# Kernel optimization log

Measured on AMD Instinct MI355X. Metric: run time of the kernel, lower is better.

The kernel has to match this reference:

```python
import jax, jax.numpy as jnp
import numpy as np

DIM = 128
SUPPORT = 1
NL, NM, NG = 5, 20, 100
EPS_BN = 1e-5
EPS_NORM = 1e-12


def knn_idx(vertices, k):
    # vertices: (b, v, 3) -> (b, v, k) indices of k nearest (excluding self)
    sq = jnp.sum(vertices * vertices, axis=-1)  # (b, v)
    dist = -2.0 * jnp.einsum('bic,bjc->bij', vertices, vertices) + sq[:, :, None] + sq[:, None, :]
    _, idx = jax.lax.top_k(-dist, k + 1)  # smallest distances
    return idx[:, :, 1:]


def gather_nbr(t, idx):
    # t: (b, v, c), idx: (b, v, n) -> (b, v, n, c)
    b = t.shape[0]
    return t[jnp.arange(b)[:, None, None], idx]


def conv_layer(idx, vertices, fmap, W, bias, dirs):
    # idx: (b,v,n); fmap: (b,v,DIM); W: (DIM,(S+1)*DIM); bias: ((S+1)*DIM,); dirs: (3,S*DIM)
    nbrs = gather_nbr(vertices, idx)                      # (b,v,n,3)
    d = nbrs - vertices[:, :, None, :]
    d = d / jnp.maximum(jnp.linalg.norm(d, axis=-1, keepdims=True), EPS_NORM)
    sd = dirs / jnp.maximum(jnp.linalg.norm(dirs, axis=0, keepdims=True), EPS_NORM)
    theta = jax.nn.relu(jnp.einsum('bvnc,ck->bvnk', d, sd))  # (b,v,n,S*DIM)
    fo = fmap @ W + bias                                   # (b,v,(S+1)*DIM)
    center = fo[..., :DIM]
    supp = gather_nbr(fo[..., DIM:], idx)                  # (b,v,n,S*DIM)
    b_, v_, n_ = idx.shape
    act = (theta * supp).reshape(b_, v_, n_, SUPPORT, DIM)
    act = jnp.max(act, axis=2).sum(axis=2)                 # max over neighbors, sum over supports
    return center + act                                    # (b,v,DIM)


def bn_relu(x, gamma, beta):
    # training-mode BatchNorm1d over (batch, points) per channel, then ReLU
    mu = jnp.mean(x, axis=(0, 1))
    var = jnp.var(x, axis=(0, 1))
    return jax.nn.relu((x - mu) * jax.lax.rsqrt(var + EPS_BN) * gamma + beta)


def setup_inputs() -> dict:
    key = jax.random.key(0)
    ks = jax.random.split(key, 8)
    B, V = 2, 1024
    return {
        'vertices': jax.random.normal(ks[0], (B, V, 3), jnp.float32),
        'x': jax.random.normal(ks[1], (B, V, DIM), jnp.float32),
        'conv_W': jax.random.normal(ks[2], (6, DIM, (SUPPORT + 1) * DIM), jnp.float32) * 0.05,
        'conv_b': jax.random.normal(ks[3], (6, (SUPPORT + 1) * DIM), jnp.float32) * 0.05,
        'conv_dirs': jax.random.normal(ks[4], (6, 3, SUPPORT * DIM), jnp.float32),
        'bn_gamma': jnp.ones((6, DIM), jnp.float32),
        'bn_beta': jnp.zeros((6, DIM), jnp.float32),
        'down_W': jax.random.normal(ks[5], (3 * DIM, 2 * DIM), jnp.float32) * 0.05,
        'down_b': jax.random.normal(ks[6], (2 * DIM,), jnp.float32) * 0.05,
    }


def reference(vertices, x, conv_W, conv_b, conv_dirs, bn_gamma, bn_beta, down_W, down_b):
    il = knn_idx(vertices, NL)
    im = knn_idx(vertices, NM)
    ig = knn_idx(vertices, NG)
    # param index order: 0=l, 1=m0, 2=m1, 3=g0, 4=g1, 5=g2 (g2 unused, per source bug)
    fl = bn_relu(conv_layer(il, vertices, x, conv_W[0], conv_b[0], conv_dirs[0]), bn_gamma[0], bn_beta[0])
    fm = bn_relu(conv_layer(im, vertices, x, conv_W[1], conv_b[1], conv_dirs[1]), bn_gamma[1], bn_beta[1])
    fm = bn_relu(conv_layer(im, vertices, fm, conv_W[2], conv_b[2], conv_dirs[2]), bn_gamma[2], bn_beta[2])
    fg = bn_relu(conv_layer(ig, vertices, x, conv_W[3], conv_b[3], conv_dirs[3]), bn_gamma[3], bn_beta[3])
    fg = bn_relu(conv_layer(ig, vertices, fg, conv_W[4], conv_b[4], conv_dirs[4]), bn_gamma[4], bn_beta[4])
    # source reuses conv_g0 / bn_g0 for the third global layer
    fg = bn_relu(conv_layer(ig, vertices, fg, conv_W[3], conv_b[3], conv_dirs[3]), bn_gamma[3], bn_beta[3])
    out = jnp.concatenate([fl, fm, fg], axis=2)            # (b, v, 3*DIM)
    return jax.nn.relu(out @ down_W + down_b)              # (b, v, 2*DIM)
```

## Files before the change

### kernel.cpp

```cpp
#include <hip/hip_runtime.h>


__device__ __forceinline__ void do_gemm(
    const float* __restrict__ in, const float* __restrict__ stp,
    const float* __restrict__ gm, const float* __restrict__ bt,
    const float* __restrict__ W, const float* __restrict__ bi,
    float* __restrict__ out, int rb, char* smemc)
{
    float* rows  = (float*)smemc;
    float* wch   = rows + 1024;
    float* scale = wch + 4096;
    float* shift = scale + 128;
    int t = threadIdx.x;
    if (t < 128) {
        float sc = 1.0f, sf = 0.0f;
        if (stp) {
            float sm = 0.0f, sq = 0.0f;
            #pragma unroll 8
            for (int bk = 0; bk < 32; ++bk) {
                sm += stp[bk*256 + t];
                sq += stp[bk*256 + 128 + t];
            }
            float mu  = sm * (1.0f/2048.0f);
            float var = sq * (1.0f/2048.0f) - mu*mu;
            sc = rsqrtf(var + 1e-5f) * gm[t];
            sf = bt[t] - mu*sc;
        }
        scale[t] = sc; shift[t] = sf;
    }
    __syncthreads();
    int r0 = rb * 8;
    {
        float4 v = ((const float4*)(in + r0*128))[t];
        if (stp) {
            int c4 = (t & 31) << 2;
            v.x = fmaxf(v.x*scale[c4  ] + shift[c4  ], 0.0f);
            v.y = fmaxf(v.y*scale[c4+1] + shift[c4+1], 0.0f);
            v.z = fmaxf(v.z*scale[c4+2] + shift[c4+2], 0.0f);
            v.w = fmaxf(v.w*scale[c4+3] + shift[c4+3], 0.0f);
        }
        ((float4*)rows)[t] = v;
    }
    int cb = t & 63, rp = (t >> 6) << 1;
    const float* a0r = rows + rp*128;
    const float* a1r = a0r + 128;
    const float4* W4 = (const float4*)W;
    float4* wch4 = (float4*)wch;
    float4 acc0 = make_float4(0.f,0.f,0.f,0.f);
    float4 acc1 = make_float4(0.f,0.f,0.f,0.f);
    for (int c = 0; c < 8; ++c) {
        __syncthreads();
        #pragma unroll
        for (int i = 0; i < 4; ++i)
            wch4[t + 256*i] = W4[c*1024 + t + 256*i];
        __syncthreads();
        int kb = c*16;
        #pragma unroll
        for (int k = 0; k < 16; k += 4) {
            float4 a0 = *(const float4*)(a0r + kb + k);
            float4 a1 = *(const float4*)(a1r + kb + k);
            float4 w;
            w = wch4[(k+0)*64+cb];
            acc0.x += a0.x*w.x; acc0.y += a0.x*w.y; acc0.z += a0.x*w.z; acc0.w += a0.x*w.w;
            acc1.x += a1.x*w.x; acc1.y += a1.x*w.y; acc1.z += a1.x*w.z; acc1.w += a1.x*w.w;
            w = wch4[(k+1)*64+cb];
            acc0.x += a0.y*w.x; acc0.y += a0.y*w.y; acc0.z += a0.y*w.z; acc0.w += a0.y*w.w;
            acc1.x += a1.y*w.x; acc1.y += a1.y*w.y; acc1.z += a1.y*w.z; acc1.w += a1.y*w.w;
            w = wch4[(k+2)*64+cb];
            acc0.x += a0.z*w.x; acc0.y += a0.z*w.y; acc0.z += a0.z*w.z; acc0.w += a0.z*w.w;
            acc1.x += a1.z*w.x; acc1.y += a1.z*w.y; acc1.z += a1.z*w.z; acc1.w += a1.z*w.w;
            w = wch4[(k+3)*64+cb];
            acc0.x += a0.w*w.x; acc0.y += a0.w*w.y; acc0.z += a0.w*w.z; acc0.w += a0.w*w.w;
            acc1.x += a1.w*w.x; acc1.y += a1.w*w.y; acc1.z += a1.w*w.z; acc1.w += a1.w*w.w;
        }
    }
    float4 b4 = ((const float4*)bi)[cb];
    acc0.x += b4.x; acc0.y += b4.y; acc0.z += b4.z; acc0.w += b4.w;
    acc1.x += b4.x; acc1.y += b4.y; acc1.z += b4.z; acc1.w += b4.w;
    ((float4*)out)[(r0+rp  )*64 + cb] = acc0;
    ((float4*)out)[(r0+rp+1)*64 + cb] = acc1;
}

__device__ __forceinline__ void do_gemm_big(
    const float* __restrict__ in, const float* __restrict__ stp,
    const float* __restrict__ gm, const float* __restrict__ bt,
    const float* __restrict__ W, const float* __restrict__ bi,
    float* __restrict__ out, int rb, char* smemc)
{
    float* rows  = (float*)smemc;
    float* wch   = rows + 1024;
    float* scale = wch + 16384;
    float* shift = scale + 128;
    int t = threadIdx.x;
    if (t < 128) {
        float sc = 1.0f, sf = 0.0f;
        if (stp) {
            float sm = 0.0f, sq = 0.0f;
            #pragma unroll 8
            for (int bk = 0; bk < 32; ++bk) {
                sm += stp[bk*256 + t];
                sq += stp[bk*256 + 128 + t];
            }
            float mu  = sm * (1.0f/2048.0f);
            float var = sq * (1.0f/2048.0f) - mu*mu;
            sc = rsqrtf(var + 1e-5f) * gm[t];
            sf = bt[t] - mu*sc;
        }
        scale[t] = sc; shift[t] = sf;
    }
    __syncthreads();
    int r0 = rb * 8;
    {
        float4 v = ((const float4*)(in + r0*128))[t];
        if (stp) {
            int c4 = (t & 31) << 2;
            v.x = fmaxf(v.x*scale[c4  ] + shift[c4  ], 0.0f);
            v.y = fmaxf(v.y*scale[c4+1] + shift[c4+1], 0.0f);
            v.z = fmaxf(v.z*scale[c4+2] + shift[c4+2], 0.0f);
            v.w = fmaxf(v.w*scale[c4+3] + shift[c4+3], 0.0f);
        }
        ((float4*)rows)[t] = v;
    }
    int cb = t & 63, rp = (t >> 6) << 1;
    const float* a0r = rows + rp*128;
    const float* a1r = a0r + 128;
    const float4* W4 = (const float4*)W;
    float4* wch4 = (float4*)wch;
    float4 acc0 = make_float4(0.f,0.f,0.f,0.f);
    float4 acc1 = make_float4(0.f,0.f,0.f,0.f);
    for (int c = 0; c < 2; ++c) {
        __syncthreads();
        #pragma unroll
        for (int i = 0; i < 16; ++i)
            wch4[t + 256*i] = W4[c*4096 + t + 256*i];
        __syncthreads();
        int kb = c*64;
        #pragma unroll 4
        for (int k = 0; k < 64; k += 4) {
            float4 a0 = *(const float4*)(a0r + kb + k);
            float4 a1 = *(const float4*)(a1r + kb + k);
            float4 w;
            w = wch4[(k+0)*64+cb];
            acc0.x += a0.x*w.x; acc0.y += a0.x*w.y; acc0.z += a0.x*w.z; acc0.w += a0.x*w.w;
            acc1.x += a1.x*w.x; acc1.y += a1.x*w.y; acc1.z += a1.x*w.z; acc1.w += a1.x*w.w;
            w = wch4[(k+1)*64+cb];
            acc0.x += a0.y*w.x; acc0.y += a0.y*w.y; acc0.z += a0.y*w.z; acc0.w += a0.y*w.w;
            acc1.x += a1.y*w.x; acc1.y += a1.y*w.y; acc1.z += a1.y*w.z; acc1.w += a1.y*w.w;
            w = wch4[(k+2)*64+cb];
            acc0.x += a0.z*w.x; acc0.y += a0.z*w.y; acc0.z += a0.z*w.z; acc0.w += a0.z*w.w;
            acc1.x += a1.z*w.x; acc1.y += a1.z*w.y; acc1.z += a1.z*w.z; acc1.w += a1.z*w.w;
            w = wch4[(k+3)*64+cb];
            acc0.x += a0.w*w.x; acc0.y += a0.w*w.y; acc0.z += a0.w*w.z; acc0.w += a0.w*w.w;
            acc1.x += a1.w*w.x; acc1.y += a1.w*w.y; acc1.z += a1.w*w.z; acc1.w += a1.w*w.w;
        }
    }
    float4 b4 = ((const float4*)bi)[cb];
    acc0.x += b4.x; acc0.y += b4.y; acc0.z += b4.z; acc0.w += b4.w;
    acc1.x += b4.x; acc1.y += b4.y; acc1.z += b4.z; acc1.w += b4.w;
    ((float4*)out)[(r0+rp  )*64 + cb] = acc0;
    ((float4*)out)[(r0+rp+1)*64 + cb] = acc1;
}

__global__ void k1_kernel(const float* __restrict__ verts, const float* __restrict__ dirs,
                          const float* __restrict__ x,
                          const float* __restrict__ convW, const float* __restrict__ convB,
                          int* __restrict__ idxout, float* __restrict__ sdn,
                          float* __restrict__ stp, float* __restrict__ fo)
{
    __shared__ __align__(16) char smem[21504];
    int t = threadIdx.x;
    int blk = blockIdx.x;

    if (blk >= 1280) {
        if (blk == 1472) {
            for (int i = t; i < 768; i += 256) {
                int l = i >> 7, k = i & 127;
                float a = dirs[l*384 + k];
                float b = dirs[l*384 + 128 + k];
                float c = dirs[l*384 + 256 + k];
                float nrm = sqrtf(a*a + b*b + c*c);
                float inv = 1.0f / fmaxf(nrm, 1e-12f);
                sdn[l*384 + k]       = a*inv;
                sdn[l*384 + 128 + k] = b*inv;
                sdn[l*384 + 256 + k] = c*inv;
            }
        } else {
            stp[(blk - 1280)*256 + t] = 0.0f;
        }
        return;
    }
    if (blk >= 512) {
        int g = blk - 512;
        int s = g >> 8, rb = g & 255;
        int wi = (s==0) ? 0 : (s==1) ? 1 : 3;
        do_gemm(x, (const float*)0, (const float*)0, (const float*)0,
                convW + wi*32768, convB + wi*256, fo + s*524288, rb, smem);
        return;
    }

    float* xs  = (float*)smem;
    float* ys  = xs + 1024;
    float* zs  = ys + 1024;
    float* sqs = zs + 1024;
    unsigned int* histBase = (unsigned int*)(smem + 16384);
    unsigned int* selBase  = (unsigned int*)(smem + 20480);

    int w = t >> 6, l = t & 63;
    int vglob = blk*4 + w;
    int b = vglob >> 10;
    int v = vglob & 1023;
    unsigned long long* keys = (unsigned long long*)smem + w*256;
    unsigned int* hist = histBase + w*256;
    unsigned int* sel  = selBase + w*4;

    const float* vb = verts + b * 3072;
    for (int i = t; i < 1024; i += 256) {
        float xx = vb[i*3+0], yy = vb[i*3+1], zz = vb[i*3+2];
        xs[i] = xx; ys[i] = yy; zs[i] = zz;
        sqs[i] = xx*xx + yy*yy + zz*zz;
    }
    __syncthreads();

    float cx = xs[v], cy = ys[v], cz = zs[v], csq = sqs[v];
    unsigned long long K16[16];
    #pragma unroll
    for (int q = 0; q < 16; ++q) {
        int j = q*64 + l;
        float dot = cx*xs[j] + cy*ys[j] + cz*zs[j];
        float d = -2.0f*dot + csq + sqs[j];
        unsigned int u = __float_as_uint(d);
        u = (u & 0x80000000u) ? ~u : (u | 0x80000000u);
        K16[q] = (((unsigned long long)u) << 32) | (unsigned long long)j;
    }
    #pragma unroll
    for (int i = 0; i < 4; ++i) hist[l*4 + i] = 0u;
    __syncthreads();

    #pragma unroll
    for (int q = 0; q < 16; ++q)
        atomicAdd(&hist[(unsigned int)(K16[q] >> 56)], 1u);
    __syncthreads();

    {
        unsigned int h0 = hist[l*4], h1 = hist[l*4+1], h2 = hist[l*4+2], h3 = hist[l*4+3];
        unsigned int c1 = h0, c2 = h0+h1, c3 = h0+h1+h2, T = c3+h3;
        unsigned int xacc = T;
        #pragma unroll
        for (int off = 1; off < 64; off <<= 1) {
            unsigned int y = __shfl_up(xacc, off, 64);
            if (l >= off) xacc += y;
        }
        unsigned int P = xacc - T;
        unsigned int ex[4] = {P, P+c1, P+c2, P+c3};
        unsigned int hh[4] = {h0, h1, h2, h3};
        #pragma unroll
        for (int i = 0; i < 4; ++i) {
            if (ex[i] < 101u && ex[i] + hh[i] >= 101u) {
                sel[0] = (unsigned int)(l*4 + i);
                sel[1] = 101u - ex[i];
            }
        }
    }
    __syncthreads();
    unsigned int P8 = sel[0], rank2 = sel[1];
    #pragma unroll
    for (int i = 0; i < 4; ++i) hist[l*4 + i] = 0u;
    __syncthreads();

    #pragma unroll
    for (int q = 0; q < 16; ++q)
        if ((unsigned int)(K16[q] >> 56) == P8)
            atomicAdd(&hist[(unsigned int)(K16[q] >> 48) & 0xFFu], 1u);
    __syncthreads();

    {
        unsigned int h0 = hist[l*4], h1 = hist[l*4+1], h2 = hist[l*4+2], h3 = hist[l*4+3];
        unsigned int c1 = h0, c2 = h0+h1, c3 = h0+h1+h2, T = c3+h3;
        unsigned int xacc = T;
        #pragma unroll
        for (int off = 1; off < 64; off <<= 1) {
            unsigned int y = __shfl_up(xacc, off, 64);
            if (l >= off) xacc += y;
        }
        unsigned int P = xacc - T;
        unsigned int ex[4] = {P, P+c1, P+c2, P+c3};
        unsigned int hh[4] = {h0, h1, h2, h3};
        #pragma unroll
        for (int i = 0; i < 4; ++i) {
            if (ex[i] < rank2 && ex[i] + hh[i] >= rank2) {
                sel[2] = (P8 << 8) | (unsigned int)(l*4 + i);
                sel[3] = 0u;
            }
        }
    }
    __syncthreads();
    unsigned int P16 = sel[2];

    #pragma unroll
    for (int q = 0; q < 16; ++q) {
        if ((unsigned int)(K16[q] >> 48) <= P16) {
            unsigned int pos = atomicAdd(&sel[3], 1u);
            if (pos < 256u) keys[pos] = K16[q];
        }
    }
    __syncthreads();
    unsigned int cnt = sel[3];

    unsigned long long K[4];
    #pragma unroll
    for (int q = 0; q < 4; ++q) {
        unsigned int e = (unsigned int)(l*4 + q);
        K[q] = (e < cnt) ? keys[e] : 0xFFFFFFFFFFFFFFFFULL;
    }

    auto cswap = [&](int qa, int qb, int k) {
        int e = (l << 2) + qa;
        bool up = ((e & k) == 0);
        unsigned long long a = K[qa], bb2 = K[qb];
        unsigned long long mn = a < bb2 ? a : bb2;
        unsigned long long mx = a < bb2 ? bb2 : a;
        K[qa] = up ? mn : mx;
        K[qb] = up ? mx : mn;
    };
    #pragma unroll
    for (int k = 2; k <= 256; k <<= 1) {
        for (int j = k >> 1; j >= 4; j >>= 1) {
            int lj = j >> 2;
            #pragma unroll
            for (int q = 0; q < 4; ++q) {
                unsigned long long other = __shfl_xor(K[q], lj, 64);
                int e = (l << 2) + q;
                bool up = ((e & k) == 0);
                bool lower = ((l & lj) == 0);
                bool takeMin = (lower == up);
                unsigned long long mn = K[q] < other ? K[q] : other;
                unsigned long long mx = K[q] < other ? other : K[q];
                K[q] = takeMin ? mn : mx;
            }
        }
        if (k >= 4) { cswap(0, 2, k); cswap(1, 3, k); }
        cswap(0, 1, k); cswap(2, 3, k);
    }

    #pragma unroll
    for (int q = 0; q < 4; ++q) {
        int e = l*4 + q;
        if (e >= 1 && e <= 100)
            idxout[vglob*100 + (e-1)] = (int)(K[q] & 0xFFFFFFFFu);
    }
}

__global__ void agg_kernel(const int* __restrict__ idx, const float* __restrict__ verts,
                           const float* __restrict__ sdn, const float* __restrict__ fo,
                           int n0, int n1, int n2, int d0, int d1, int d2,
                           float* o0, float* o1, float* o2,
                           float* s0p, float* s1p, float* s2p)
{
    __shared__ float4 ds4s[200];
    __shared__ int jss[200];
    int slot = blockIdx.y;
    int n  = slot==0 ? n0 : slot==1 ? n1 : n2;
    int dI = slot==0 ? d0 : slot==1 ? d1 : d2;
    float* outp = slot==0 ? o0 : slot==1 ? o1 : o2;
    float* stp  = slot==0 ? s0p : slot==1 ? s1p : s2p;
    const float* fos = fo + slot * 524288;
    const float* sd = sdn + dI * 384;

    int t = threadIdx.x;
    int h = t >> 7, tt = t & 127;
    float4* ds4 = ds4s + h*100;
    int* js = jss + h*100;
    int r = blockIdx.x*2 + h;
    int b = r >> 10;

    if (tt < n) {
        int j = idx[r*100 + tt];
        js[tt] = j;
        const float* pj = verts + (b*1024 + j)*3;
        const float* pv = verts + r*3;
        float dx = pj[0]-pv[0], dy = pj[1]-pv[1], dz = pj[2]-pv[2];
        float nm = sqrtf(dx*dx + dy*dy + dz*dz);
        float inv = 1.0f / fmaxf(nm, 1e-12f);
        ds4[tt] = make_float4(dx*inv, dy*inv, dz*inv, 0.0f);
    }
    __syncthreads();
    float s0 = sd[tt], s1 = sd[128+tt], s2 = sd[256+tt];
    int bb = b * 1024;
    float m = -3.0e38f;
    for (int q = 0; q < n; q += 5) {
        float th[5];
        const float* p[5];
        #pragma unroll
        for (int u = 0; u < 5; ++u) {
            float4 dq = ds4[q+u];
            th[u] = fmaxf(dq.x*s0 + dq.y*s1 + dq.z*s2, 0.0f);
            p[u] = fos + (size_t)(bb + js[q+u])*256 + 128 + tt;
        }
        float vv[5];
        #pragma unroll
        for (int u = 0; u < 5; ++u) vv[u] = *p[u];
        #pragma unroll
        for (int u = 0; u < 5; ++u) m = fmaxf(m, th[u]*vv[u]);
    }
    float val = fos[r*256 + tt] + m;
    outp[r*128 + tt] = val;
    float* bank = stp + (r & 31)*256;
    atomicAdd(&bank[tt], val);
    atomicAdd(&bank[128+tt], val*val);
}

__global__ void gemm2_kernel(
    const float* inA, const float* stA, const float* gA, const float* beA,
    const float* WA, const float* biA, float* foA,
    const float* inB, const float* stB, const float* gB, const float* beB,
    const float* WB, const float* biB, float* foB)
{
    __shared__ __align__(16) char smem[70656];
    if (blockIdx.y == 0)
        do_gemm_big(inA, stA, gA, beA, WA, biA, foA, blockIdx.x, smem);
    else
        do_gemm_big(inB, stB, gB, beB, WB, biB, foB, blockIdx.x, smem);
}

__global__ void down_kernel(
    const float* __restrict__ p0, const float* __restrict__ s0p,
    const float* __restrict__ g0, const float* __restrict__ be0,
    const float* __restrict__ p1, const float* __restrict__ s1p,
    const float* __restrict__ g1, const float* __restrict__ be1,
    const float* __restrict__ p2, const float* __restrict__ s2p,
    const float* __restrict__ g2, const float* __restrict__ be2,
    const float* __restrict__ dW, const float* __restrict__ db,
    float* __restrict__ out)
{
    __shared__ __align__(16) float rows[16*384];
    __shared__ __align__(16) float4 wch4[4096];
    __shared__ float scale[384], shift[384];
    int t = threadIdx.x;
    int r0 = blockIdx.x * 16;
    int colblk = blockIdx.y;

    for (int c = t; c < 384; c += 256) {
        int seg = c >> 7, cc = c & 127;
        const float* stp = seg==0 ? s0p : seg==1 ? s1p : s2p;
        const float* g   = seg==0 ? g0  : seg==1 ? g1  : g2;
        const float* be  = seg==0 ? be0 : seg==1 ? be1 : be2;
        float sm = 0.0f, sq = 0.0f;
        #pragma unroll 8
        for (int bk = 0; bk < 32; ++bk) {
            sm += stp[bk*256 + cc];
            sq += stp[bk*256 + 128 + cc];
        }
        float mu  = sm * (1.0f/2048.0f);
        float var = sq * (1.0f/2048.0f) - mu*mu;
        float s = rsqrtf(var + 1e-5f) * g[cc];
        scale[c] = s;
        shift[c] = be[cc] - mu*s;
    }
    __syncthreads();
    for (int q = t; q < 1536; q += 256) {
        int row = q / 96, rem = q - row*96;
        int c4 = rem << 2;
        int seg = c4 >> 7, cc = c4 & 127;
        const float* ps = seg==0 ? p0 : seg==1 ? p1 : p2;
        float4 v = *(const float4*)(ps + (r0+row)*128 + cc);
        v.x = fmaxf(v.x*scale[c4  ] + shift[c4  ], 0.0f);
        v.y = fmaxf(v.y*scale[c4+1] + shift[c4+1], 0.0f);
        v.z = fmaxf(v.z*scale[c4+2] + shift[c4+2], 0.0f);
        v.w = fmaxf(v.w*scale[c4+3] + shift[c4+3], 0.0f);
        *(float4*)&rows[row*384 + c4] = v;
    }

    int cb = t & 31;
    int rg = t >> 5;
    const float* a0r = rows + (rg*2)*384;
    const float* a1r = a0r + 384;
    const float4* W4 = (const float4*)dW;
    float4 acc0 = make_float4(0.f,0.f,0.f,0.f);
    float4 acc1 = make_float4(0.f,0.f,0.f,0.f);
    for (int c = 0; c < 3; ++c) {
        __syncthreads();
        #pragma unroll
        for (int i = 0; i < 16; ++i) {
            int e = t + 256*i;
            wch4[e] = W4[c*8192 + colblk*32 + (e >> 5)*64 + (e & 31)];
        }
        __syncthreads();
        int kb = c*128;
        #pragma unroll 8
        for (int k = 0; k < 128; k += 4) {
            float4 a0 = *(const float4*)(a0r + kb + k);
            float4 a1 = *(const float4*)(a1r + kb + k);
            float4 w;
            w = wch4[(k+0)*32+cb];
            acc0.x += a0.x*w.x; acc0.y += a0.x*w.y; acc0.z += a0.x*w.z; acc0.w += a0.x*w.w;
            acc1.x += a1.x*w.x; acc1.y += a1.x*w.y; acc1.z += a1.x*w.z; acc1.w += a1.x*w.w;
            w = wch4[(k+1)*32+cb];
            acc0.x += a0.y*w.x; acc0.y += a0.y*w.y; acc0.z += a0.y*w.z; acc0.w += a0.y*w.w;
            acc1.x += a1.y*w.x; acc1.y += a1.y*w.y; acc1.z += a1.y*w.z; acc1.w += a1.y*w.w;
            w = wch4[(k+2)*32+cb];
            acc0.x += a0.z*w.x; acc0.y += a0.z*w.y; acc0.z += a0.z*w.z; acc0.w += a0.z*w.w;
            acc1.x += a1.z*w.x; acc1.y += a1.z*w.y; acc1.z += a1.z*w.z; acc1.w += a1.z*w.w;
            w = wch4[(k+3)*32+cb];
            acc0.x += a0.w*w.x; acc0.y += a0.w*w.y; acc0.z += a0.w*w.z; acc0.w += a0.w*w.w;
            acc1.x += a1.w*w.x; acc1.y += a1.w*w.y; acc1.z += a1.w*w.z; acc1.w += a1.w*w.w;
        }
    }
    float4 b4 = ((const float4*)db)[colblk*32 + cb];
    float4 o0, o1;
    o0.x = fmaxf(acc0.x + b4.x, 0.0f); o0.y = fmaxf(acc0.y + b4.y, 0.0f);
    o0.z = fmaxf(acc0.z + b4.z, 0.0f); o0.w = fmaxf(acc0.w + b4.w, 0.0f);
    o1.x = fmaxf(acc1.x + b4.x, 0.0f); o1.y = fmaxf(acc1.y + b4.y, 0.0f);
    o1.z = fmaxf(acc1.z + b4.z, 0.0f); o1.w = fmaxf(acc1.w + b4.w, 0.0f);
    ((float4*)out)[(r0 + rg*2    )*64 + colblk*32 + cb] = o0;
    ((float4*)out)[(r0 + rg*2 + 1)*64 + colblk*32 + cb] = o1;
}

extern "C" void kernel_launch(void* const* d_in, const int* in_sizes, int n_in,
                              void* d_out, int out_size, void* d_ws, size_t ws_size,
                              hipStream_t stream)
{
    (void)in_sizes; (void)n_in; (void)out_size; (void)ws_size;
    const float* verts = (const float*)d_in[0];
    const float* x     = (const float*)d_in[1];
    const float* convW = (const float*)d_in[2];
    const float* convB = (const float*)d_in[3];
    const float* dirs  = (const float*)d_in[4];
    const float* gam   = (const float*)d_in[5];
    const float* bet   = (const float*)d_in[6];
    const float* dW    = (const float*)d_in[7];
    const float* db    = (const float*)d_in[8];
    float* out = (float*)d_out;

    char* ws = (char*)d_ws;
    int*   idxb = (int*)(ws);
    float* sdn  = (float*)(ws + 819200);
    float* stp  = (float*)(ws + 828416);
    float* fo   = (float*)(ws + 1025024);
    float* p0   = (float*)(ws + 7316480);
    float* p1   = (float*)(ws + 8365056);
    float* p2   = (float*)(ws + 9413632);
    float* p3   = (float*)(ws + 10462208);
    float* p4   = (float*)(ws + 11510784);
    float* p5   = (float*)(ws + 12559360);

    const float* nf = (const float*)0;
    float* nw = (float*)0;
    float* stL0 = stp,         *stL1 = stp + 8192, *stL2 = stp + 16384;
    float* stL3 = stp + 24576, *stL4 = stp + 32768, *stL5 = stp + 40960;

    k1_kernel<<<1473, 256, 0, stream>>>(verts, dirs, x, convW, convB,
                                        idxb, sdn, stp, fo);
    agg_kernel<<<dim3(1024,3), 256, 0, stream>>>(
        idxb, verts, sdn, fo, 5, 20, 100, 0, 1, 3,
        p0, p1, p3, stL0, stL1, stL3);
    gemm2_kernel<<<dim3(256,2), 256, 0, stream>>>(
        p1, stL1, gam + 128, bet + 128, convW + 65536,  convB + 512,  fo,
        p3, stL3, gam + 384, bet + 384, convW + 131072, convB + 1024, fo + 524288);
    agg_kernel<<<dim3(1024,2), 256, 0, stream>>>(
        idxb, verts, sdn, fo, 20, 100, 0, 2, 4, 0,
        p2, p4, nw, stL2, stL4, nw);
    gemm2_kernel<<<dim3(256,1), 256, 0, stream>>>(
        p4, stL4, gam + 512, bet + 512, convW + 98304, convB + 768, fo,
        nf, nf, nf, nf, nf, nf, nw);
    agg_kernel<<<dim3(1024,1), 256, 0, stream>>>(
        idxb, verts, sdn, fo, 100, 0, 0, 3, 0, 0,
        p5, nw, nw, stL5, nw, nw);
    down_kernel<<<dim3(128,2), 256, 0, stream>>>(
        p0, stL0, gam, bet,
        p2, stL2, gam + 256, bet + 256,
        p5, stL5, gam + 384, bet + 384,
        dW, db, out);
}
```

Measured before the change: 178.1 us.

## Vectorize neighbor gather with float4 and split neighbors across thread groups

The aggregation kernel now has each thread handle four channels through float4 loads and split the neighbor list across four groups of 32 threads. Partial maxima are combined through a shared-memory reduction. Neighbor offsets are precomputed as row*256 in shared memory. The aim is fewer, wider gather loads and more memory-level parallelism per thread, at the cost of an extra barrier, a shared reduction, and masked tail iterations when n is not a multiple of 20.

New measurement: 201.3 us. 13.1% more time.

```diff
diff --git a/kernel.cpp b/kernel.cpp
--- a/kernel.cpp
+++ b/kernel.cpp
@@ -358,6 +358,7 @@
 {
     __shared__ float4 ds4s[200];
     __shared__ int jss[200];
+    __shared__ float4 redm[2][4][32];
     int slot = blockIdx.y;
     int n  = slot==0 ? n0 : slot==1 ? n1 : n2;
     int dI = slot==0 ? d0 : slot==1 ? d1 : d2;
@@ -372,41 +373,83 @@
     int* js = jss + h*100;
     int r = blockIdx.x*2 + h;
     int b = r >> 10;
+    int bb = b * 1024;
 
     if (tt < n) {
         int j = idx[r*100 + tt];
-        js[tt] = j;
-        const float* pj = verts + (b*1024 + j)*3;
+        const float* pj = verts + (bb + j)*3;
         const float* pv = verts + r*3;
         float dx = pj[0]-pv[0], dy = pj[1]-pv[1], dz = pj[2]-pv[2];
         float nm = sqrtf(dx*dx + dy*dy + dz*dz);
         float inv = 1.0f / fmaxf(nm, 1e-12f);
         ds4[tt] = make_float4(dx*inv, dy*inv, dz*inv, 0.0f);
-    }
-    __syncthreads();
-    float s0 = sd[tt], s1 = sd[128+tt], s2 = sd[256+tt];
-    int bb = b * 1024;
-    float m = -3.0e38f;
-    for (int q = 0; q < n; q += 5) {
-        float th[5];
-        const float* p[5];
+        js[tt] = (bb + j) << 8;
+    }
+    __syncthreads();
+
+    int c = tt & 31, g = tt >> 5;
+    int c4 = c << 2;
+    float4 S0 = *(const float4*)(sd + c4);
+    float4 S1 = *(const float4*)(sd + 128 + c4);
+    float4 S2 = *(const float4*)(sd + 256 + c4);
+
+    float4 m4 = make_float4(-3.0e38f, -3.0e38f, -3.0e38f, -3.0e38f);
+    for (int q = g; q < n; q += 20) {
+        float4 th[5]; int off[5]; bool ok[5];
         #pragma unroll
         for (int u = 0; u < 5; ++u) {
-            float4 dq = ds4[q+u];
-            th[u] = fmaxf(dq.x*s0 + dq.y*s1 + dq.z*s2, 0.0f);
-            p[u] = fos + (size_t)(bb + js[q+u])*256 + 128 + tt;
-        }
-        float vv[5];
-        #pragma unroll
-        for (int u = 0; u < 5; ++u) vv[u] = *p[u];
-        #pragma unroll
-        for (int u = 0; u < 5; ++u) m = fmaxf(m, th[u]*vv[u]);
-    }
-    float val = fos[r*256 + tt] + m;
-    outp[r*128 + tt] = val;
-    float* bank = stp + (r & 31)*256;
-    atomicAdd(&bank[tt], val);
-    atomicAdd(&bank[128+tt], val*val);
+            int qq = q + u*4;
+            ok[u] = (qq < n);
+            int qs = ok[u] ? qq : g;
+            float4 dq = ds4[qs];
+            th[u].x = fmaxf(dq.x*S0.x + dq.y*S1.x + dq.z*S2.x, 0.0f);
+            th[u].y = fmaxf(dq.x*S0.y + dq.y*S1.y + dq.z*S2.y, 0.0f);
+            th[u].z = fmaxf(dq.x*S0.z + dq.y*S1.z + dq.z*S2.z, 0.0f);
+            th[u].w = fmaxf(dq.x*S0.w + dq.y*S1.w + dq.z*S2.w, 0.0f);
+            off[u] = js[qs];
+        }
+        float4 vv[5];
+        #pragma unroll
+        for (int u = 0; u < 5; ++u)
+            vv[u] = *(const float4*)(fos + off[u] + 128 + c4);
+        #pragma unroll
+        for (int u = 0; u < 5; ++u) {
+            if (ok[u]) {
+                m4.x = fmaxf(m4.x, th[u].x*vv[u].x);
+                m4.y = fmaxf(m4.y, th[u].y*vv[u].y);
+                m4.z = fmaxf(m4.z, th[u].z*vv[u].z);
+                m4.w = fmaxf(m4.w, th[u].w*vv[u].w);
+            }
+        }
+    }
+    redm[h][g][c] = m4;
+    __syncthreads();
+    if (g < 2) {
+        float4 aa = redm[h][0][c], bq = redm[h][1][c];
+        float4 cq = redm[h][2][c], dq2 = redm[h][3][c];
+        float4 mm;
+        mm.x = fmaxf(fmaxf(aa.x,bq.x), fmaxf(cq.x,dq2.x));
+        mm.y = fmaxf(fmaxf(aa.y,bq.y), fmaxf(cq.y,dq2.y));
+        mm.z = fmaxf(fmaxf(aa.z,bq.z), fmaxf(cq.z,dq2.z));
+        mm.w = fmaxf(fmaxf(aa.w,bq.w), fmaxf(cq.w,dq2.w));
+        float4 ctr = *(const float4*)(fos + r*256 + c4);
+        float4 val;
+        val.x = ctr.x + mm.x; val.y = ctr.y + mm.y;
+        val.z = ctr.z + mm.z; val.w = ctr.w + mm.w;
+        if (g == 0) {
+            *(float4*)(outp + r*128 + c4) = val;
+        } else {
+            float* bank = stp + (r & 31)*256;
+            atomicAdd(&bank[c4+0], val.x);
+            atomicAdd(&bank[c4+1], val.y);
+            atomicAdd(&bank[c4+2], val.z);
+            atomicAdd(&bank[c4+3], val.w);
+            atomicAdd(&bank[128+c4+0], val.x*val.x);
+            atomicAdd(&bank[128+c4+1], val.y*val.y);
+            atomicAdd(&bank[128+c4+2], val.z*val.z);
+            atomicAdd(&bank[128+c4+3], val.w*val.w);
+        }
+    }
 }
 
 __global__ void gemm2_kernel(
```
